# Kernel tuning notes

Measured on AMD Instinct MI355X. Metric: run time of the kernel, lower is better.

## Reference

```python
import jax, jax.numpy as jnp
import numpy as np

B, T, N, D = 32, 336, 321, 3
G = 512          # global_hidden
L = 2            # layer_nums
E = 4            # experts per layer
K = 2            # top-k
F = 2048         # d_ff (expert hidden)
P = 96           # pred_len
LOSS_COEF = 0.01


def setup_inputs() -> dict:
    key = jax.random.key(0)
    ks = iter(jax.random.split(key, 24))
    rn = lambda shape, s=0.02: jax.random.normal(next(ks), shape, jnp.float32) * s
    return {
        "x": jax.random.normal(next(ks), (B, T, N, D), jnp.float32),
        # GlobalEmbedding
        "Wv": rn((N, 1)), "bv": jnp.zeros((1,), jnp.float32),
        "Wt": rn((T, G)), "bt": jnp.zeros((G,), jnp.float32),
        # CrossAttention
        "Wq": rn((G, G)), "bq": jnp.zeros((G,), jnp.float32),
        "Wk": rn((G, G)), "bk": jnp.zeros((G,), jnp.float32),
        "Wva": rn((G, G)), "bva": jnp.zeros((G,), jnp.float32),
        # AMS MoE layers (stacked over L)
        "Wg": rn((L, T, E)),
        "We1": rn((L, E, T, F)), "be1": jnp.zeros((L, E, F), jnp.float32),
        "We2": rn((L, E, F, T)), "be2": jnp.zeros((L, E, T), jnp.float32),
        # projections head
        "P1w": rn((T, P)), "P1b": jnp.zeros((P,), jnp.float32),
        "P2w": rn((P, 2 * P)), "P2b": jnp.zeros((2 * P,), jnp.float32),
    }


def _cv_squared(v):
    return v.var() / (v.mean() ** 2 + 1e-10)


def reference(x, Wv, bv, Wt, bt, Wq, bq, Wk, bk, Wva, bva,
              Wg, We1, be1, We2, be2, P1w, P1b, P2w, P2b):
    Bv, Tv, Nv, Dv = x.shape
    # ---- GlobalEmbedding: (B,T,N,D) -> (B,D,G), with the original's raw reshape
    g = jnp.einsum('btvd,vo->btdo', x, Wv)[..., 0] + bv[0]        # (B,T,D)
    g2 = g.reshape(Bv * Dv, Tv) @ Wt + bt                          # faithful contiguous reshape
    gf = g2.reshape(Bv, Dv, -1)                                    # (B,D,G)
    # ---- CrossAttention (no sqrt(d) scaling, per source)
    q = gf @ Wq + bq
    kk = gf @ Wk + bk
    v = gf @ Wva + bva
    attn = jax.nn.softmax(jnp.einsum('big,bjg->bij', q, kk), axis=-1)
    sst_attended = jnp.einsum('bij,bjg->big', attn, v)[:, 0, :]    # unused: use_attend=0
    del sst_attended
    # ---- slice value channel + RevIN norm over time
    x0 = x[..., 0]                                                 # (B,T,N)
    mu = x0.mean(axis=1, keepdims=True)
    sd = jnp.sqrt(x0.var(axis=1, keepdims=True) + 1e-5)
    out = (x0 - mu) / sd
    # ---- AMS layers: clean top-k gated MoE over per-node seq MLP experts
    balance_loss = jnp.float32(0.0)
    for l in range(L):
        logits = out.mean(axis=2) @ Wg[l]                          # (B,E)
        topv, topi = jax.lax.top_k(logits, K)
        gates = jnp.zeros_like(logits).at[
            jnp.arange(Bv)[:, None], topi].set(jax.nn.softmax(topv, axis=-1))
        importance = gates.sum(axis=0)
        balance_loss = balance_loss + _cv_squared(importance) * LOSS_COEF
        xt = out.transpose(0, 2, 1)                                # (B,N,T)
        h = jax.nn.relu(jnp.einsum('bnt,etf->ebnf', xt, We1[l])
                        + be1[l][:, None, None, :])                # (E,B,N,F)
        eo = jnp.einsum('ebnf,eft->ebnt', h, We2[l]) + be2[l][:, None, None, :]
        moe = jnp.einsum('be,ebnt->bnt', gates, eo).transpose(0, 2, 1)
        out = out + moe                                            # residual_connection=1
    # ---- projection head
    o = out.transpose(0, 2, 1)                                     # (B,N,T)
    hproj = jnp.tanh(o @ P1w + P1b)
    p = (hproj @ P2w + P2b).reshape(Bv, Nv, P, 2).transpose(0, 2, 1, 3)  # (B,P,N,2)
    mean = p[..., 0]
    std = jax.nn.softplus(p[..., 1]) + 1e-6
    return mean, balance_loss, std
```

## Files before the change

### kernel.cpp

```cpp
#include <hip/hip_runtime.h>
#include <hip/hip_bf16.h>
#include <cstdint>
#include <math.h>

#define B_ 32
#define T_ 336
#define N_ 321
#define L_ 2
#define E_ 4
#define F_ 2048
#define P_ 96
#define TPAD 352
#define NPAD 384

typedef __hip_bfloat16 bf16;
typedef __attribute__((ext_vector_type(8))) __bf16 bf16x8;
typedef __attribute__((ext_vector_type(4))) float f32x4;


__device__ __forceinline__ void async_copy16(const void* g, void* l) {
  __builtin_amdgcn_global_load_lds(
      (__attribute__((address_space(1))) void*)(uintptr_t)g,
      (__attribute__((address_space(3))) void*)(unsigned int)(uintptr_t)l,
      16, 0, 0);
}

__device__ __forceinline__ void pipe_barrier_vm0() {
  asm volatile("s_waitcnt vmcnt(0)" ::: "memory");
  __builtin_amdgcn_s_barrier();
  __builtin_amdgcn_sched_barrier(0);
}

__device__ __forceinline__ void pipe_barrier_full() {
  asm volatile("s_waitcnt vmcnt(0) lgkmcnt(0)" ::: "memory");
  __builtin_amdgcn_s_barrier();
  __builtin_amdgcn_sched_barrier(0);
}

__global__ void transpose_cast_kernel(const float* __restrict__ src, bf16* __restrict__ dst,
                                      int R, int C, int Rp, int Cp,
                                      long long sStride, long long dStride) {
  __shared__ float tile[32][33];
  const float* s = src + (size_t)blockIdx.z * sStride;
  bf16* d = dst + (size_t)blockIdx.z * dStride;
  int r0 = blockIdx.x * 32, c0 = blockIdx.y * 32;
  int tx = threadIdx.x, ty = threadIdx.y;
  #pragma unroll
  for (int ii = 0; ii < 4; ii++) {
    int rl = ty * 4 + ii;
    int r = r0 + rl, c = c0 + tx;
    tile[rl][tx] = (r < R && c < C) ? s[(size_t)r * C + c] : 0.f;
  }
  __syncthreads();
  #pragma unroll
  for (int ii = 0; ii < 4; ii++) {
    int cl = ty * 4 + ii;
    int cd = c0 + cl, rd = r0 + tx;
    if (cd < Cp && rd < Rp)
      d[(size_t)cd * Rp + rd] = __float2bfloat16(tile[tx][cl]);
  }
}

__global__ void repack_w2_kernel(const float* __restrict__ src, bf16* __restrict__ dst) {
  __shared__ float tile[32][96];
  int le = blockIdx.z, tb = blockIdx.y, f0 = blockIdx.x * 32;
  int tid = threadIdx.x;
  const float* s = src + (size_t)le * F_ * T_;
  for (int idx = tid; idx < 32 * 96; idx += 256) {
    int ff = idx / 96, tt = idx % 96;
    int t = tb * 96 + tt;
    tile[ff][tt] = (t < T_) ? s[(size_t)(f0 + ff) * T_ + t] : 0.f;
  }
  __syncthreads();
  bf16* d = dst + ((size_t)le * 4 + tb) * 196608 + (size_t)(f0 >> 3) * 768;
  for (int s2 = tid; s2 < 384; s2 += 256) {
    int kgl = s2 / 96, row = s2 % 96;
    bf16 v[8];
    #pragma unroll
    for (int j = 0; j < 8; j++) v[j] = __float2bfloat16(tile[kgl * 8 + j][row]);
    *(uint4*)(d + (size_t)kgl * 768 + row * 8) = *(const uint4*)v;
  }
}

__global__ __launch_bounds__(512) void revin_kernel(const float* __restrict__ x,
                                                    float* __restrict__ out,
                                                    bf16* __restrict__ Abuf) {
  __shared__ float red[8][64][2];
  __shared__ float minv[64][2];
  __shared__ unsigned int Lt[64][177];

  const int b = blockIdx.x;
  const int n0 = blockIdx.y * 64;
  const int tid = threadIdx.x;
  const int nl = tid & 63, tq = tid >> 6;
  const int n = n0 + nl;
  const bool valid = (n < N_);
  const float* xp = x + ((size_t)b * T_ * N_ + n) * 3;
  const int tbeg = tq * 42, tend = tbeg + 42;

  float s1 = 0.f, s2 = 0.f;
  if (valid) {
    for (int t = tbeg; t < tend; t++) {
      float v = xp[(size_t)t * N_ * 3];
      s1 += v; s2 += v * v;
    }
  }
  red[tq][nl][0] = s1; red[tq][nl][1] = s2;
  __syncthreads();
  if (tid < 64) {
    float a = 0.f, c = 0.f;
    #pragma unroll
    for (int q = 0; q < 8; q++) { a += red[q][tid][0]; c += red[q][tid][1]; }
    float mu = a / (float)T_;
    float var = c / (float)T_ - mu * mu;
    minv[tid][0] = mu;
    minv[tid][1] = 1.f / sqrtf(var + 1e-5f);
  }
  {
    int r = tid >> 3, c = 168 + (tid & 7);
    Lt[r][c] = 0u;
  }
  __syncthreads();

  const float mu = minv[nl][0], inv = minv[nl][1];
  for (int t = tbeg; t < tend; t += 2) {
    float v0 = 0.f, v1 = 0.f;
    if (valid) {
      v0 = (xp[(size_t)t * N_ * 3] - mu) * inv;
      v1 = (xp[(size_t)(t + 1) * N_ * 3] - mu) * inv;
      out[((size_t)b * T_ + t) * N_ + n] = v0;
      out[((size_t)b * T_ + t + 1) * N_ + n] = v1;
    }
    bf16 h0 = __float2bfloat16(v0), h1 = __float2bfloat16(v1);
    unsigned int u = (unsigned int)*(unsigned short*)&h0 |
                     ((unsigned int)*(unsigned short*)&h1 << 16);
    Lt[nl][t >> 1] = u;
  }
  __syncthreads();

  unsigned int* abase = (unsigned int*)(Abuf + ((size_t)b * NPAD + n0) * TPAD);
  #pragma unroll
  for (int k = 0; k < 22; k++) {
    int idx = tid + k * 512;
    int row = idx / 176, c = idx % 176;
    abase[(size_t)row * (TPAD / 2) + c] = Lt[row][c];
  }
}

__global__ void gate1_kernel(const float* __restrict__ out, float* __restrict__ colsum) {
  int b = blockIdx.y;
  int w = threadIdx.x >> 6, lane = threadIdx.x & 63;
  int t = blockIdx.x * 16 + w * 4;
  #pragma unroll
  for (int i = 0; i < 4; i++, t++) {
    const float* p = out + ((size_t)b * T_ + t) * N_;
    float s = 0.f;
    for (int n = lane; n < N_; n += 64) s += p[n];
    #pragma unroll
    for (int off = 32; off; off >>= 1) s += __shfl_down(s, off);
    if (lane == 0) colsum[b * T_ + t] = s;
  }
}

__global__ void gate2_kernel(const float* __restrict__ colsum, const float* __restrict__ Wg,
                             int* __restrict__ pair_e, float* __restrict__ pair_gate,
                             float* __restrict__ loss_partial, int layer) {
  __shared__ float lg[32][4];
  __shared__ float gates[32][4];
  __shared__ float imp[4];
  int tid = threadIdx.x;
  if (tid < 128) {
    int b = tid >> 2, e = tid & 3;
    float s = 0.f;
    for (int t = 0; t < T_; t++)
      s += colsum[b * T_ + t] * Wg[(layer * T_ + t) * E_ + e];
    lg[b][e] = s / (float)N_;
  }
  __syncthreads();
  if (tid < 32) {
    float v[4];
    #pragma unroll
    for (int e = 0; e < 4; e++) v[e] = lg[tid][e];
    int i0 = 0;
    for (int e = 1; e < 4; e++) if (v[e] > v[i0]) i0 = e;
    int i1 = -1;
    for (int e = 0; e < 4; e++) {
      if (e == i0) continue;
      if (i1 < 0 || v[e] > v[i1]) i1 = e;
    }
    float ex = expf(v[i1] - v[i0]);
    float g0 = 1.f / (1.f + ex);
    float g1 = ex / (1.f + ex);
    pair_e[tid * 2] = i0; pair_e[tid * 2 + 1] = i1;
    pair_gate[tid * 2] = g0; pair_gate[tid * 2 + 1] = g1;
    #pragma unroll
    for (int e = 0; e < 4; e++) gates[tid][e] = 0.f;
    gates[tid][i0] = g0; gates[tid][i1] = g1;
  }
  __syncthreads();
  if (tid < 4) {
    float s = 0.f;
    for (int bb = 0; bb < 32; bb++) s += gates[bb][tid];
    imp[tid] = s;
  }
  __syncthreads();
  if (tid == 0) {
    float m = (imp[0] + imp[1] + imp[2] + imp[3]) * 0.25f;
    float va = 0.f;
    #pragma unroll
    for (int e = 0; e < 4; e++) { float d = imp[e] - m; va += d * d; }
    va *= 0.25f;
    loss_partial[layer] = 0.01f * (va / (m * m + 1e-10f));
  }
}

__global__ __launch_bounds__(256) void gemm1_kernel(
    const bf16* __restrict__ Abuf, const bf16* __restrict__ W1T,
    const float* __restrict__ be1, const int* __restrict__ pair_e,
    const float* __restrict__ pair_gate, bf16* __restrict__ h, int layer) {
  __shared__ __align__(16) bf16 S1[16384];
  __shared__ float bias_s[128];

  const int tid = threadIdx.x;
  const int w = tid >> 6, lane = tid & 63;
  const int pair = blockIdx.z;
  const int b = pair >> 1;
  const int e = pair_e[pair];
  const float gate = pair_gate[pair];
  const int m0 = blockIdx.y * 128;
  const int f0 = blockIdx.x * 128;

  const bf16* Ag = Abuf + (size_t)b * NPAD * TPAD + (size_t)m0 * TPAD;
  const bf16* Bg = W1T + ((size_t)(layer * E_ + e) * F_ + f0) * TPAD;
  if (tid < 128) bias_s[tid] = be1[(size_t)(layer * E_ + e) * F_ + f0 + tid];

  f32x4 acc[4][4];
  const f32x4 zero = {0.f, 0.f, 0.f, 0.f};
  #pragma unroll
  for (int i = 0; i < 4; i++)
    #pragma unroll
    for (int j = 0; j < 4; j++) acc[i][j] = zero;

  const int wm = w >> 1, wn = w & 1;
  const int lrow = lane >> 2;
  const int lkoff = (lane & 3) * 8;
  const int quad = lane >> 4;
  const int l15 = lane & 15;

  auto stage1 = [&](int k, int buf) {
    const int k0 = k * 32;
    bf16* As = S1 + buf * 8192;
    bf16* Bs = As + 4096;
    #pragma unroll
    for (int i = 0; i < 2; i++) {
      int r = (w * 2 + i) * 16 + lrow;
      async_copy16(Ag + (size_t)r * TPAD + k0 + lkoff, As + (w * 2 + i) * 512);
      async_copy16(Bg + (size_t)r * TPAD + k0 + lkoff, Bs + (w * 2 + i) * 512);
    }
  };

  stage1(0, 0);
  pipe_barrier_full();

  for (int kk = 0; kk < TPAD / 32; ++kk) {
    if (kk < TPAD / 32 - 1) stage1(kk + 1, (kk + 1) & 1);
    const bf16* As = S1 + (kk & 1) * 8192;
    const bf16* Bs = As + 4096;
    bf16x8 af[4], bfr[4];
    #pragma unroll
    for (int mi = 0; mi < 4; mi++)
      af[mi] = *(const bf16x8*)(As + (wm * 64 + mi * 16 + l15) * 32 + quad * 8);
    #pragma unroll
    for (int ni = 0; ni < 4; ni++)
      bfr[ni] = *(const bf16x8*)(Bs + (wn * 64 + ni * 16 + l15) * 32 + quad * 8);
    #pragma unroll
    for (int mi = 0; mi < 4; mi++)
      #pragma unroll
      for (int ni = 0; ni < 4; ni++)
        acc[mi][ni] = __builtin_amdgcn_mfma_f32_16x16x32_bf16(af[mi], bfr[ni], acc[mi][ni], 0, 0, 0);
    pipe_barrier_vm0();
  }

  bf16* tw0 = S1 + w * 1024;
  bf16* tw1 = S1 + 4096 + w * 1024;
  size_t hb = (size_t)pair * 786432 + (size_t)((m0 >> 6) + wm) * 131072;
  const int kgbase = (f0 >> 3) + wn * 8 + (lane & 3) * 2;
  #pragma unroll
  for (int mi = 0; mi < 4; mi++) {
    bf16* tw = (mi & 1) ? tw1 : tw0;
    #pragma unroll
    for (int ni = 0; ni < 4; ni++) {
      float bias = bias_s[wn * 64 + ni * 16 + l15];
      #pragma unroll
      for (int r = 0; r < 4; r++) {
        float v = acc[mi][ni][r] + bias;
        v = fmaxf(v, 0.f) * gate;
        tw[(quad * 4 + r) * 64 + ni * 16 + l15] = __float2bfloat16(v);
      }
    }
    int row = lane >> 2;
    int fpart = (lane & 3) * 16;
    const uint4* sp = (const uint4*)(tw + row * 64 + fpart);
    uint4 d0 = sp[0];
    uint4 d1 = sp[1];
    bf16* dp = h + hb + (size_t)kgbase * 512 + (mi * 16 + row) * 8;
    *(uint4*)dp = d0;
    *(uint4*)(dp + 512) = d1;
  }
}

#define CT_STRIDE 104
__global__ __launch_bounds__(256) void gemm2_kernel(
    const bf16* __restrict__ h, const bf16* __restrict__ W2B,
    const float* __restrict__ be2, const int* __restrict__ pair_e,
    const float* __restrict__ pair_gate, float* __restrict__ out,
    bf16* __restrict__ Abuf, int layer) {
  __shared__ __align__(16) bf16 S[20480];
  __shared__ float bias_t[96];

  const int tid = threadIdx.x;
  const int w = tid >> 6, lane = tid & 63;
  const int id = blockIdx.x;
  const int u = id & 7;
  const int v = id >> 3;
  const int tt = v & 3;
  const int pn = u + 8 * (v >> 2);
  const int b = pn / 6, nt = pn % 6;
  const int n0 = nt * 64, t0 = tt * 96;

  const int e0 = pair_e[b * 2], e1 = pair_e[b * 2 + 1];
  const float g0 = pair_gate[b * 2], g1 = pair_gate[b * 2 + 1];
  const bf16* Agb0 = h + ((size_t)(b * 2) * 6 + nt) * 131072;
  const bf16* Agb1 = h + ((size_t)(b * 2 + 1) * 6 + nt) * 131072;
  const bf16* Bgb0 = W2B + ((size_t)(layer * E_ + e0) * 4 + tt) * 196608;
  const bf16* Bgb1 = W2B + ((size_t)(layer * E_ + e1) * 4 + tt) * 196608;
  const int quad = lane >> 4, l15 = lane & 15;
  const int wm = w >> 1, wt = w & 1;

  if (tid < 96) {
    int t = t0 + tid;
    bias_t[tid] = (t < T_)
        ? g0 * be2[(layer * E_ + e0) * T_ + t] + g1 * be2[(layer * E_ + e1) * T_ + t]
        : 0.f;
  }

  f32x4 acc[2][3];
  const f32x4 zero = {0.f, 0.f, 0.f, 0.f};
  #pragma unroll
  for (int i = 0; i < 2; i++)
    #pragma unroll
    for (int jj = 0; jj < 3; jj++) acc[i][jj] = zero;

  auto stage2 = [&](int k, int buf) {
    const bf16* Aj = ((k < 32) ? Agb0 : Agb1) + (size_t)(k & 31) * 4096;
    const bf16* Bj = ((k < 32) ? Bgb0 : Bgb1) + (size_t)(k & 31) * 6144;
    bf16* As2 = S + buf * 10240;
    bf16* Bs2 = As2 + 4096;
    #pragma unroll
    for (int i = 0; i < 2; i++)
      async_copy16(Aj + (w * 2 + i) * 512 + lane * 8, As2 + (w * 2 + i) * 512);
    #pragma unroll
    for (int i = 0; i < 3; i++)
      async_copy16(Bj + (w * 3 + i) * 512 + lane * 8, Bs2 + (w * 3 + i) * 512);
  };

  stage2(0, 0);
  pipe_barrier_full();

  for (int kk = 0; kk < 64; ++kk) {
    if (kk < 63) stage2(kk + 1, (kk + 1) & 1);
    const bf16* As2 = S + (kk & 1) * 10240;
    const bf16* Bs2 = As2 + 4096;
    #pragma unroll
    for (int w32 = 0; w32 < 2; w32++) {
      const int kg = w32 * 4 + quad;
      bf16x8 af[2], bfr[3];
      #pragma unroll
      for (int mi = 0; mi < 2; mi++)
        af[mi] = *(const bf16x8*)(As2 + kg * 512 + (wm * 32 + mi * 16 + l15) * 8);
      #pragma unroll
      for (int ni = 0; ni < 3; ni++)
        bfr[ni] = *(const bf16x8*)(Bs2 + kg * 768 + (wt * 48 + ni * 16 + l15) * 8);
      #pragma unroll
      for (int mi = 0; mi < 2; mi++)
        #pragma unroll
        for (int ni = 0; ni < 3; ni++)
          acc[mi][ni] = __builtin_amdgcn_mfma_f32_16x16x32_bf16(af[mi], bfr[ni], acc[mi][ni], 0, 0, 0);
    }
    pipe_barrier_vm0();
  }

  #pragma unroll
  for (int mi = 0; mi < 2; mi++) {
    #pragma unroll
    for (int ni = 0; ni < 3; ni++) {
      int nloc_b = wm * 32 + mi * 16 + quad * 4;
      int tloc = wt * 48 + ni * 16 + l15;
      int t = t0 + tloc;
      #pragma unroll
      for (int r = 0; r < 4; r++) {
        int nloc = nloc_b + r;
        int n = n0 + nloc;
        float vv = 0.f;
        if (n < N_ && t < T_) {
          size_t q = ((size_t)b * T_ + t) * N_ + n;
          vv = out[q] + acc[mi][ni][r] + bias_t[tloc];
          out[q] = vv;
        }
        S[nloc * CT_STRIDE + tloc] = __float2bfloat16(vv);
      }
    }
  }
  __syncthreads();
  #pragma unroll
  for (int it = 0; it < 3; ++it) {
    int idx = tid + it * 256;
    int row = idx / 12, seg = idx % 12;
    int t = t0 + seg * 8;
    if (t < TPAD)
      *(uint4*)(Abuf + ((size_t)b * NPAD + n0 + row) * TPAD + t) =
          *(const uint4*)(S + row * CT_STRIDE + seg * 8);
  }
}

#define HS_STRIDE 104
__global__ __launch_bounds__(256) void proj_kernel(
    const bf16* __restrict__ Abuf, const bf16* __restrict__ P1T, const float* __restrict__ P1b,
    const bf16* __restrict__ P2T, const float* __restrict__ P2b,
    const float* __restrict__ loss_partial, float* __restrict__ dout) {
  __shared__ __align__(16) bf16 Hs[64 * HS_STRIDE];
  const int tid = threadIdx.x;
  const int w = tid >> 6, lane = tid & 63;
  const int quad = lane >> 4, l15 = lane & 15;
  const int b = blockIdx.y;
  const int m0 = blockIdx.x * 64;
  const int row = w * 16;

  f32x4 acc1[6];
  const f32x4 zero = {0.f, 0.f, 0.f, 0.f};
  #pragma unroll
  for (int j = 0; j < 6; j++) acc1[j] = zero;

  const bf16* Arow = Abuf + ((size_t)b * NPAD + m0 + row) * TPAD;
  for (int kk = 0; kk < TPAD / 32; ++kk) {
    bf16x8 af, bfr[6];
    af = *(const bf16x8*)(Arow + (size_t)l15 * TPAD + kk * 32 + quad * 8);
    #pragma unroll
    for (int ni = 0; ni < 6; ni++)
      bfr[ni] = *(const bf16x8*)(P1T + (size_t)(ni * 16 + l15) * TPAD + kk * 32 + quad * 8);
    #pragma unroll
    for (int ni = 0; ni < 6; ni++)
      acc1[ni] = __builtin_amdgcn_mfma_f32_16x16x32_bf16(af, bfr[ni], acc1[ni], 0, 0, 0);
  }

  #pragma unroll
  for (int ni = 0; ni < 6; ni++) {
    float bias = P1b[ni * 16 + l15];
    #pragma unroll
    for (int r = 0; r < 4; r++) {
      float x = acc1[ni][r] + bias;
      float t = 1.f - 2.f / (__expf(2.f * x) + 1.f);
      Hs[(row + quad * 4 + r) * HS_STRIDE + ni * 16 + l15] = __float2bfloat16(t);
    }
  }
  __syncthreads();

  #pragma unroll
  for (int half = 0; half < 2; ++half) {
    f32x4 acc2[6];
    #pragma unroll
    for (int j = 0; j < 6; j++) acc2[j] = zero;

    #pragma unroll
    for (int kk = 0; kk < 3; ++kk) {
      bf16x8 af, bfr[6];
      af = *(const bf16x8*)(Hs + (row + l15) * HS_STRIDE + kk * 32 + quad * 8);
      #pragma unroll
      for (int ni = 0; ni < 6; ni++)
        bfr[ni] = *(const bf16x8*)(P2T + (size_t)((half * 6 + ni) * 16 + l15) * P_ + kk * 32 + quad * 8);
      #pragma unroll
      for (int ni = 0; ni < 6; ni++)
        acc2[ni] = __builtin_amdgcn_mfma_f32_16x16x32_bf16(af, bfr[ni], acc2[ni], 0, 0, 0);
    }

    #pragma unroll
    for (int ni = 0; ni < 6; ni++) {
      int jj = (half * 6 + ni) * 16 + l15;
      float bias = P2b[jj];
      int pout = jj >> 1;
      #pragma unroll
      for (int r = 0; r < 4; r++) {
        int n = m0 + row + quad * 4 + r;
        if (n < N_) {
          float s = acc2[ni][r] + bias;
          size_t o = ((size_t)b * P_ + pout) * N_ + n;
          if ((jj & 1) == 0) {
            dout[o] = s;
          } else {
            float sp = (s > 20.f) ? s : log1pf(__expf(s));
            dout[(size_t)B_ * P_ * N_ + 1 + o] = sp + 1e-6f;
          }
        }
      }
    }
  }
  if (b == 0 && blockIdx.x == 0 && tid == 0)
    dout[(size_t)B_ * P_ * N_] = loss_partial[0] + loss_partial[1];
}

extern "C" void kernel_launch(void* const* d_in, const int* in_sizes, int n_in,
                              void* d_out, int out_size, void* d_ws, size_t ws_size,
                              hipStream_t stream) {
  const float* x   = (const float*)d_in[0];
  const float* Wg  = (const float*)d_in[11];
  const float* We1 = (const float*)d_in[12];
  const float* be1 = (const float*)d_in[13];
  const float* We2 = (const float*)d_in[14];
  const float* be2 = (const float*)d_in[15];
  const float* P1w = (const float*)d_in[16];
  const float* P1b = (const float*)d_in[17];
  const float* P2w = (const float*)d_in[18];
  const float* P2b = (const float*)d_in[19];

  char* ws = (char*)d_ws;
  size_t off = 0;
  auto alloc = [&](size_t bytes) -> void* {
    void* p = ws + off;
    off += (bytes + 255) & ~(size_t)255;
    return p;
  };
  float* out        = (float*)alloc((size_t)B_ * T_ * N_ * 4);
  bf16*  Abuf       = (bf16*) alloc((size_t)B_ * NPAD * TPAD * 2);
  bf16*  W1T        = (bf16*) alloc((size_t)L_ * E_ * F_ * TPAD * 2);
  bf16*  W2B        = (bf16*) alloc((size_t)L_ * E_ * 4 * 196608 * 2);
  bf16*  P1T        = (bf16*) alloc((size_t)P_ * TPAD * 2);
  bf16*  P2T        = (bf16*) alloc((size_t)2 * P_ * P_ * 2);
  bf16*  h          = (bf16*) alloc((size_t)B_ * 2 * 786432 * 2);
  float* colsum     = (float*)alloc((size_t)B_ * T_ * 4);
  int*   pair_e     = (int*)  alloc(B_ * 2 * 4);
  float* pair_gate  = (float*)alloc(B_ * 2 * 4);
  float* loss_part  = (float*)alloc(2 * 4);
  if (ws_size < off) return;

  dim3 tb(32, 8);
  transpose_cast_kernel<<<dim3(11, 64, 8), tb, 0, stream>>>(
      We1, W1T, T_, F_, TPAD, F_, (long long)T_ * F_, (long long)F_ * TPAD);
  repack_w2_kernel<<<dim3(64, 4, 8), 256, 0, stream>>>(We2, W2B);
  transpose_cast_kernel<<<dim3(11, 3, 1), tb, 0, stream>>>(
      P1w, P1T, T_, P_, TPAD, P_, 0, 0);
  transpose_cast_kernel<<<dim3(3, 6, 1), tb, 0, stream>>>(
      P2w, P2T, P_, 2 * P_, P_, 2 * P_, 0, 0);

  revin_kernel<<<dim3(B_, 6), 512, 0, stream>>>(x, out, Abuf);

  for (int l = 0; l < L_; ++l) {
    gate1_kernel<<<dim3(21, B_), 256, 0, stream>>>(out, colsum);
    gate2_kernel<<<1, 128, 0, stream>>>(colsum, Wg, pair_e, pair_gate, loss_part, l);
    gemm1_kernel<<<dim3(16, 3, 64), 256, 0, stream>>>(Abuf, W1T, be1, pair_e, pair_gate, h, l);
    gemm2_kernel<<<768, 256, 0, stream>>>(h, W2B, be2, pair_e, pair_gate, out, Abuf, l);
  }

  proj_kernel<<<dim3(6, B_), 256, 0, stream>>>(Abuf, P1T, P1b, P2T, P2b, loss_part,
                                               (float*)d_out);
}
```

Baseline: 527.7 us.

## Deepen gemm2 pipeline with triple-buffered A and partial vmcnt waits

```diff
diff --git a/kernel.cpp b/kernel.cpp
--- a/kernel.cpp
+++ b/kernel.cpp
@@ -36,6 +36,13 @@
   __builtin_amdgcn_s_barrier();
   __builtin_amdgcn_sched_barrier(0);
 }
+
+#define G2_WAITN(N)                                         \
+  do {                                                      \
+    asm volatile("s_waitcnt vmcnt(" #N ")" ::: "memory");   \
+    __builtin_amdgcn_s_barrier();                           \
+    __builtin_amdgcn_sched_barrier(0);                      \
+  } while (0)
 
 __global__ void transpose_cast_kernel(const float* __restrict__ src, bf16* __restrict__ dst,
                                       int R, int C, int Rp, int Cp,
@@ -315,7 +322,7 @@
     const float* __restrict__ be2, const int* __restrict__ pair_e,
     const float* __restrict__ pair_gate, float* __restrict__ out,
     bf16* __restrict__ Abuf, int layer) {
-  __shared__ __align__(16) bf16 S[20480];
+  __shared__ __align__(16) bf16 S[24576];
   __shared__ float bias_t[96];
 
   const int tid = threadIdx.x;
@@ -343,6 +350,7 @@
         ? g0 * be2[(layer * E_ + e0) * T_ + t] + g1 * be2[(layer * E_ + e1) * T_ + t]
         : 0.f;
   }
+  pipe_barrier_full();
 
   f32x4 acc[2][3];
   const f32x4 zero = {0.f, 0.f, 0.f, 0.f};
@@ -351,26 +359,24 @@
     #pragma unroll
     for (int jj = 0; jj < 3; jj++) acc[i][jj] = zero;
 
-  auto stage2 = [&](int k, int buf) {
-    const bf16* Aj = ((k < 32) ? Agb0 : Agb1) + (size_t)(k & 31) * 4096;
-    const bf16* Bj = ((k < 32) ? Bgb0 : Bgb1) + (size_t)(k & 31) * 6144;
-    bf16* As2 = S + buf * 10240;
-    bf16* Bs2 = As2 + 4096;
-    #pragma unroll
-    for (int i = 0; i < 2; i++)
-      async_copy16(Aj + (w * 2 + i) * 512 + lane * 8, As2 + (w * 2 + i) * 512);
-    #pragma unroll
-    for (int i = 0; i < 3; i++)
-      async_copy16(Bj + (w * 3 + i) * 512 + lane * 8, Bs2 + (w * 3 + i) * 512);
+  const int aoff = w * 1024 + lane * 8;
+  const int boff = w * 1536 + lane * 8;
+
+  auto stageA = [&](const bf16* Aj, int buf) {
+    bf16* As2 = S + buf * 4096;
+    async_copy16(Aj + aoff, As2 + w * 1024);
+    async_copy16(Aj + aoff + 512, As2 + w * 1024 + 512);
   };
-
-  stage2(0, 0);
-  pipe_barrier_full();
-
-  for (int kk = 0; kk < 64; ++kk) {
-    if (kk < 63) stage2(kk + 1, (kk + 1) & 1);
-    const bf16* As2 = S + (kk & 1) * 10240;
-    const bf16* Bs2 = As2 + 4096;
+  auto stageB = [&](const bf16* Bj, int buf) {
+    bf16* Bs2 = S + 12288 + buf * 6144;
+    async_copy16(Bj + boff, Bs2 + w * 1536);
+    async_copy16(Bj + boff + 512, Bs2 + w * 1536 + 512);
+    async_copy16(Bj + boff + 1024, Bs2 + w * 1536 + 1024);
+  };
+
+  auto compute = [&](int bufA, int bufB) {
+    const bf16* As2 = S + bufA * 4096;
+    const bf16* Bs2 = S + 12288 + bufB * 6144;
     #pragma unroll
     for (int w32 = 0; w32 < 2; w32++) {
       const int kg = w32 * 4 + quad;
@@ -387,8 +393,53 @@
         for (int ni = 0; ni < 3; ni++)
           acc[mi][ni] = __builtin_amdgcn_mfma_f32_16x16x32_bf16(af[mi], bfr[ni], acc[mi][ni], 0, 0, 0);
     }
-    pipe_barrier_vm0();
-  }
+  };
+
+  stageB(Bgb0, 0);
+  stageA(Agb0, 0);
+  stageA(Agb0 + 4096, 1);
+  G2_WAITN(2);
+
+  const bf16* aNext = Agb0 + 2 * 4096;
+  const bf16* bNext = Bgb0 + 6144;
+
+  #pragma unroll 1
+  for (int j = 0; j < 10; ++j) {
+    const int k = j * 6;
+#define G2S(i, bB1, bA2, cA, cB)                              \
+    stageB(bNext, bB1);                                       \
+    stageA(aNext, bA2);                                       \
+    bNext = (k + (i) == 30) ? Bgb1 : bNext + 6144;            \
+    aNext = (k + (i) == 29) ? Agb1 : aNext + 4096;            \
+    compute(cA, cB);                                          \
+    G2_WAITN(2);
+    G2S(0, 1, 2, 0, 0)
+    G2S(1, 0, 0, 1, 1)
+    G2S(2, 1, 1, 2, 0)
+    G2S(3, 0, 2, 0, 1)
+    G2S(4, 1, 0, 1, 0)
+    G2S(5, 0, 1, 2, 1)
+#undef G2S
+  }
+
+  stageB(bNext, 1);
+  stageA(aNext, 2);
+  bNext += 6144; aNext += 4096;
+  compute(0, 0);
+  G2_WAITN(2);
+
+  stageB(bNext, 0);
+  stageA(aNext, 0);
+  bNext += 6144;
+  compute(1, 1);
+  G2_WAITN(2);
+
+  stageB(bNext, 1);
+  compute(2, 0);
+  G2_WAITN(0);
+
+  compute(0, 1);
+  pipe_barrier_full();
 
   #pragma unroll
   for (int mi = 0; mi < 2; mi++) {
```

Result: faster. 504.4 us (-4.4%).
